# Performance work log

Measured on AMD Instinct MI355X. Metric: run time of the kernel, lower is better.

The kernel has to match this reference:

```python
import jax, jax.numpy as jnp
import numpy as np

N_HD, N_DEL7, N_AVP, N_AVM = 100, 100, 50, 50
DT = 0.001
KAPPA_PHI, KAPPA_Y = 1.0, 1.0
AV_OFFSET = 0.0
ALPHA_TILDE = 10.0
# alpha used in the leak term inside forward():
ALPHA = ALPHA_TILDE + 0.5 * KAPPA_Y / KAPPA_PHI * 1.0 / (KAPPA_PHI + KAPPA_Y)  # 10.25
W_HD_HD_S = ALPHA_TILDE + 1.0 / (KAPPA_PHI + KAPPA_Y) - AV_OFFSET * KAPPA_Y / (KAPPA_Y + KAPPA_PHI)  # 10.5
W_HD_AV_S = np.sqrt(2.0) * KAPPA_Y / (KAPPA_Y + KAPPA_PHI)  # sqrt(2)/2
W_HD_D7_S = 1.0 / (KAPPA_PHI + KAPPA_Y)  # 0.5
W_AV_HD_S = 1.0
W_D7_HD_S = 1.0
TAU_AV = 0.01
TAU_D7 = 0.001


def _id_matr(x_to, x_from, sig):
    d = np.arccos(np.cos(x_to[:, None] - x_from[None, :]))
    M = np.exp(-0.5 * (d / sig) ** 2) / (np.sqrt(2.0 * np.pi) * sig)
    return M / M.sum(1)[0]


def _build_weights():
    p_hd = np.linspace(-np.pi, np.pi - 2 * np.pi / N_HD, N_HD)
    p_d7 = np.linspace(-np.pi, np.pi - 2 * np.pi / N_DEL7, N_DEL7)
    p_avp = np.linspace(-np.pi, np.pi - 2 * np.pi / N_AVP, N_AVP)
    p_avm = np.linspace(-np.pi, np.pi - 2 * np.pi / N_AVM, N_AVM)
    o, w0, w1 = -0.2, 0.0, 2.0
    W_HD_HD = 2.0 / N_HD * (o + np.maximum(0.0, w0 + w1 * np.cos(p_hd[:, None] - p_hd[None, :])))
    W_HD_AVplus = 2.0 / N_AVP * np.maximum(0.0, np.sin(p_hd[:, None] - p_avp[None, :] + np.pi / 4))
    W_HD_AVminus = 2.0 / N_AVM * np.maximum(0.0, -np.sin(p_hd[:, None] - p_avm[None, :] - np.pi / 4))
    W_AVplus_HD = _id_matr(p_avp, p_hd, 0.3)
    W_AVminus_HD = _id_matr(p_avm, p_hd, 0.3)
    d7w0, d7w1 = 0.5, -0.5
    W_Del7_HD = 2.0 / N_DEL7 * (d7w0 + d7w1 * np.cos(p_d7[:, None] - p_hd[None, :]))
    m0, m1 = 0.1, 0.0
    W_Del7_Del7 = 2.0 / N_DEL7 * (m0 + m1 * np.cos(p_d7[:, None] - p_d7[None, :]))
    j = np.pi / 2 * (1 - 2 * m0) / d7w0
    W_HD_Del7 = -j * _id_matr(p_hd, p_d7, 0.1)
    ws = dict(W_HD_HD=W_HD_HD, W_HD_AVplus=W_HD_AVplus, W_HD_AVminus=W_HD_AVminus,
              W_AVplus_HD=W_AVplus_HD, W_AVminus_HD=W_AVminus_HD,
              W_Del7_HD=W_Del7_HD, W_Del7_Del7=W_Del7_Del7, W_HD_Del7=W_HD_Del7)
    return {k: jnp.asarray(v, dtype=jnp.float32) for k, v in ws.items()}


def setup_inputs() -> dict:
    key = jax.random.key(0)
    k1, k2 = jax.random.split(key)
    B, S = 64, 5000
    inp = {
        'inputs': jax.random.normal(k1, (B, S, 2), dtype=jnp.float32),
        'r0': jax.random.uniform(k2, (1, B, N_HD + N_AVP + N_AVM + N_DEL7), dtype=jnp.float32),
    }
    inp.update(_build_weights())
    return inp


def reference(inputs, r0, W_HD_HD, W_HD_AVplus, W_HD_AVminus, W_AVplus_HD,
              W_AVminus_HD, W_Del7_HD, W_Del7_Del7, W_HD_Del7):
    # batch_first -> [seq, batch, 2]
    x = jnp.transpose(inputs, (1, 0, 2))
    r_HD0 = r0[0, :, :N_HD]
    r_AVp0 = r0[0, :, N_HD:N_HD + N_AVP]
    r_AVm0 = r0[0, :, N_HD + N_AVP:N_HD + N_AVP + N_AVM]
    r_D70 = r0[0, :, N_HD + N_AVP + N_AVM:]
    relu = jax.nn.relu

    def step(carry, x_t):
        r_HD, r_AVp, r_AVm, r_D7 = carry
        av = x_t[:, 1]  # [B]; HD input only feeds a dead input_term in the original
        r_HD_new = (r_HD
                    - ALPHA * r_HD * DT
                    + W_HD_HD_S * jnp.einsum('ij,bj->bi', W_HD_HD, r_HD) * DT
                    + W_HD_AV_S * jnp.einsum('ij,bj->bi', W_HD_AVplus, r_AVp) * DT
                    + W_HD_AV_S * jnp.einsum('ij,bj->bi', W_HD_AVminus, r_AVm) * DT
                    + W_HD_D7_S * jnp.einsum('ij,bj->bi', W_HD_Del7, relu(r_D7)) * r_HD * DT)
        gate_p = (av / DT + AV_OFFSET)[:, None]
        gate_m = (-av / DT + AV_OFFSET)[:, None]
        r_AVp_new = r_AVp + (1.0 / TAU_AV) * (-r_AVp + gate_p * W_AV_HD_S * jnp.einsum('ij,bj->bi', W_AVplus_HD, r_HD_new)) * DT
        r_AVm_new = r_AVm + (1.0 / TAU_AV) * (-r_AVm + gate_m * W_AV_HD_S * jnp.einsum('ij,bj->bi', W_AVminus_HD, r_HD_new)) * DT
        r_D7_new = r_D7 + (1.0 / TAU_D7) * (-r_D7
                                            + W_D7_HD_S * jnp.einsum('ij,bj->bi', W_Del7_HD, relu(r_HD_new))
                                            + jnp.einsum('ij,bj->bi', W_Del7_Del7, relu(r_D7))) * DT
        out = jnp.concatenate([r_HD_new, r_AVp_new, r_AVm_new, r_D7_new], axis=1)  # [B, 300]
        return (r_HD_new, r_AVp_new, r_AVm_new, r_D7_new), out

    carry, ys = jax.lax.scan(step, (r_HD0, r_AVp0, r_AVm0, r_D70), x)
    output = jnp.transpose(ys, (1, 0, 2))  # [B, S, 300] (batch_first)
    r_full_curr = jnp.concatenate(carry, axis=1)
    return output, r_full_curr
```

## Files before the change

kernel.cpp:

```cpp
#include <hip/hip_runtime.h>


#define SSTEPS 5000
#define PI_D 3.14159265358979323846

template<int CTRL, int RM, bool BC>
__device__ __forceinline__ float dpp_mov_f(float x) {
  return __int_as_float(__builtin_amdgcn_update_dpp(0, __float_as_int(x), CTRL, RM, 0xF, BC));
}
__device__ __forceinline__ float scan16(float x) {
  x += dpp_mov_f<0x111, 0xF, true>(x);
  x += dpp_mov_f<0x112, 0xF, true>(x);
  x += dpp_mov_f<0x114, 0xF, true>(x);
  x += dpp_mov_f<0x118, 0xF, true>(x);
  return x;
}
__device__ __forceinline__ float scan8(float x) {
  x += dpp_mov_f<0x111, 0xF, true>(x);
  x += dpp_mov_f<0x112, 0xF, true>(x);
  x += dpp_mov_f<0x114, 0xF, true>(x);
  return x;
}
__device__ __forceinline__ float wave_sum(float x) {
  x = scan16(x);
  x += dpp_mov_f<0x142, 0xA, false>(x);
  x += dpp_mov_f<0x143, 0xC, false>(x);
  return __int_as_float(__builtin_amdgcn_readlane(__float_as_int(x), 63));
}

__global__ __launch_bounds__(1024, 4) void drosoph_rnn_kernel(
    const float* __restrict__ xin,
    const float* __restrict__ r0,
    const float* __restrict__ W_HD_HD,
    const float* __restrict__ W_HD_AVp,
    const float* __restrict__ W_HD_AVm,
    const float* __restrict__ W_AVp_HD,
    const float* __restrict__ W_AVm_HD,
    const float* __restrict__ W_D7_HD,
    const float* __restrict__ W_D7_D7,
    const float* __restrict__ W_HD_D7,
    float* __restrict__ out)
{
  const int b = blockIdx.x;
  const int t = threadIdx.x;

  __shared__ __align__(16) float su[2][328];
  __shared__ float avb[SSTEPS];
  __shared__ float d7r[104];

  const bool p1  = (t < 800);
  const int  g   = t >> 4;
  const int  r1  = t & 15;
  const bool pav = (t < 400);
  const int  a   = t >> 3;
  const int  qa  = t & 7;
  const bool pd7 = (t >= 832) && (t < 960);
  const int  dl  = t & 63;
  const int  o7  = t - 832;
  const bool pst = (t >= 960);

  float w1[2][20];
  if (p1) {
    #pragma unroll
    for (int k = 0; k < 2; ++k) {
      const int o = g + 50*k;
      #pragma unroll
      for (int q = 0; q < 20; ++q) {
        const int j = 20*r1 + q;
        float w;
        if      (j < 100) w = 10.5f                   * W_HD_HD [o*100 + j];
        else if (j < 150) w = 0.70710678118654752f    * W_HD_AVp[o*50 + (j-100)];
        else if (j < 200) w = 0.70710678118654752f    * W_HD_AVm[o*50 + (j-150)];
        else if (j < 300) w = 0.5f                    * W_HD_D7 [o*100 + (j-200)];
        else w = 0.0f;
        w1[k][q] = w;
      }
    }
  }

  float wav[16];
  if (pav) {
    #pragma unroll
    for (int u = 0; u < 4; ++u) {
      const int j0 = 4*(qa + 8*u);
      #pragma unroll
      for (int m = 0; m < 4; ++m) {
        const int j = j0 + m;
        wav[4*u+m] = (j < 100) ? W_AVp_HD[a*100 + j] : 0.0f;
      }
    }
  }

  float cw0=0.f, cw1=0.f, sw0=0.f, sw1=0.f, m0w=0.f, m1w=0.f, cd=0.f, sd=0.f;
  if (pd7) {
    const int j0 = 2*dl, j1 = 2*dl + 1;
    double pj0 = -PI_D + j0*(2.0*PI_D/100.0);
    double pj1 = -PI_D + j1*(2.0*PI_D/100.0);
    m0w = (j0 < 100) ? 1.0f : 0.0f;
    m1w = (j1 < 100) ? 1.0f : 0.0f;
    cw0 = m0w * (float)cos(pj0);  sw0 = m0w * (float)sin(pj0);
    cw1 = m1w * (float)cos(pj1);  sw1 = m1w * (float)sin(pj1);
    double po = -PI_D + o7*(2.0*PI_D/100.0);
    cd = (float)cos(po);  sd = (float)sin(po);
  }

  if (t < 328) { su[0][t] = 0.f; su[1][t] = 0.f; }
  if (t < 104) d7r[t] = 0.f;
  {
    const float2* x2 = (const float2*)xin + (size_t)b * SSTEPS;
    for (int i = t; i < SSTEPS; i += 1024) avb[i] = x2[i].y;
  }
  if (t < 300) {
    float v = r0[b*300 + t];
    su[0][t] = (t < 200) ? v : fmaxf(v, 0.f);
  }
  __syncthreads();

  float* outb = out + (size_t)b * ((size_t)SSTEPS * 300);
  int p = 0;

  #pragma unroll 1
  for (int s = 0; s < SSTEPS; ++s) {
    const float* suc = su[p];
    float*       sun = su[p^1];

    if (p1) {
      float vv[20];
      {
        const float4* vp = (const float4*)(suc + 20*r1);
        float4 q0=vp[0], q1=vp[1], q2=vp[2], q3=vp[3], q4=vp[4];
        *(float4*)&vv[0]=q0; *(float4*)&vv[4]=q1; *(float4*)&vv[8]=q2;
        *(float4*)&vv[12]=q3; *(float4*)&vv[16]=q4;
      }
      float hd0 = suc[g], hd1 = suc[g+50];
      float x0a=0.f, x0b=0.f, x1a=0.f, x1b=0.f;
      #pragma unroll
      for (int q = 0; q < 20; q += 2) {
        x0a = fmaf(w1[0][q],   vv[q],   x0a);
        x0b = fmaf(w1[0][q+1], vv[q+1], x0b);
        x1a = fmaf(w1[1][q],   vv[q],   x1a);
        x1b = fmaf(w1[1][q+1], vv[q+1], x1b);
      }
      float e0 = x0a + x0b, e1 = x1a + x1b;
      if (r1 >= 10) { e0 *= hd0; e1 *= hd1; }
      e0 = scan16(e0);
      e1 = scan16(e1);
      if (r1 == 15) {
        float h0 = fmaf(0.001f, fmaf(-10.25f, hd0, e0), hd0);
        float h1 = fmaf(0.001f, fmaf(-10.25f, hd1, e1), hd1);
        sun[g]    = h0;
        sun[g+50] = h1;
      }
    } else if (pst) {
      if (s > 0) {
        float* od = outb + (size_t)(s-1) * 300;
        #pragma unroll
        for (int u = 0; u < 5; ++u) {
          int idx = dl + 64*u;
          if (idx < 300) od[idx] = (idx < 200) ? suc[idx] : d7r[idx-200];
        }
      }
    }
    __syncthreads();

    if (pav) {
      const float4* hp = (const float4*)sun;
      float hh[16];
      *(float4*)&hh[0]  = hp[qa];
      *(float4*)&hh[4]  = hp[qa+8];
      *(float4*)&hh[8]  = hp[qa+16];
      *(float4*)&hh[12] = hp[qa+24];
      float da=0.f, db=0.f;
      #pragma unroll
      for (int m = 0; m < 16; m += 2) {
        da = fmaf(wav[m],   hh[m],   da);
        db = fmaf(wav[m+1], hh[m+1], db);
      }
      float d = scan8(da + db);
      if (qa == 7) {
        float av   = avb[s];
        float gp   = av / 0.001f;
        float gm   = -gp;
        float oldp = suc[100+a], oldm = suc[150+a];
        float np_  = fmaf(0.1f, fmaf(gp, d, -oldp), oldp);
        float nm_  = fmaf(0.1f, fmaf(gm, d, -oldm), oldm);
        sun[100+a] = np_;
        sun[150+a] = nm_;
      }
    }

    if (pd7) {
      float2 y2 = *(const float2*)(sun + 2*dl);
      float2 z2 = *(const float2*)(suc + 200 + 2*dl);
      float y0 = fmaxf(y2.x, 0.f), y1 = fmaxf(y2.y, 0.f);
      float pS0 = fmaf(m1w, y1,   m0w * y0);
      float pC  = fmaf(cw1, y1,   cw0 * y0);
      float pS  = fmaf(sw1, y1,   sw0 * y0);
      float pT  = fmaf(m1w, z2.y, m0w * z2.x);
      float S0 = wave_sum(pS0);
      float C  = wave_sum(pC);
      float S  = wave_sum(pS);
      float T0 = wave_sum(pT);
      if (o7 < 100) {
        float d7 = fmaf(0.002f, T0, 0.01f * (S0 - fmaf(cd, C, sd * S)));
        sun[200+o7] = fmaxf(d7, 0.f);
        d7r[o7]     = d7;
      }
    }
    __syncthreads();
    p ^= 1;
  }

  if (t < 300) {
    float v = (t < 200) ? su[p][t] : d7r[t-200];
    outb[(size_t)(SSTEPS-1) * 300 + t] = v;
    out[(size_t)64 * SSTEPS * 300 + (size_t)b * 300 + t] = v;
  }
}

extern "C" void kernel_launch(void* const* d_in, const int* in_sizes, int n_in,
                              void* d_out, int out_size, void* d_ws, size_t ws_size,
                              hipStream_t stream) {
  drosoph_rnn_kernel<<<64, 1024, 0, stream>>>(
      (const float*)d_in[0],
      (const float*)d_in[1],
      (const float*)d_in[2],
      (const float*)d_in[3],
      (const float*)d_in[4],
      (const float*)d_in[5],
      (const float*)d_in[6],
      (const float*)d_in[7],
      (const float*)d_in[8],
      (const float*)d_in[9],
      (float*)d_out);
}
```

Measured before the change: 3.979 ms.

## Move Del7 reductions off the critical path and prefetch HD state early

The HD-producing lanes now compute partial relu sums, cosine-weighted sums and sine-weighted sums of the new HD values. They reduce these by shuffles into a small shared buffer before the first barrier. As a result, the Del7 waves only combine 13 partials per quantity after the barrier instead of running four full wave reductions. The T0 reduction over previous Del7 state is moved before the first barrier as well. The HD state needed for the next step (hd and the first 100 values) is preloaded after the second phase, and the FMA chains are split into four accumulators. The extra shuffles and shared writes in phase one add some work to that phase in exchange for a shorter second phase.

After: 5.808 ms. +46.0%, slower.

```diff
diff --git a/kernel.cpp b/kernel.cpp
--- a/kernel.cpp
+++ b/kernel.cpp
@@ -9,23 +9,26 @@
   return __int_as_float(__builtin_amdgcn_update_dpp(0, __float_as_int(x), CTRL, RM, 0xF, BC));
 }
 __device__ __forceinline__ float scan16(float x) {
-  x += dpp_mov_f<0x111, 0xF, true>(x);
-  x += dpp_mov_f<0x112, 0xF, true>(x);
-  x += dpp_mov_f<0x114, 0xF, true>(x);
-  x += dpp_mov_f<0x118, 0xF, true>(x);
+  x += dpp_mov_f<0x111,0xF,true>(x);
+  x += dpp_mov_f<0x112,0xF,true>(x);
+  x += dpp_mov_f<0x114,0xF,true>(x);
+  x += dpp_mov_f<0x118,0xF,true>(x);
   return x;
 }
 __device__ __forceinline__ float scan8(float x) {
-  x += dpp_mov_f<0x111, 0xF, true>(x);
-  x += dpp_mov_f<0x112, 0xF, true>(x);
-  x += dpp_mov_f<0x114, 0xF, true>(x);
+  x += dpp_mov_f<0x111,0xF,true>(x);
+  x += dpp_mov_f<0x112,0xF,true>(x);
+  x += dpp_mov_f<0x114,0xF,true>(x);
   return x;
 }
 __device__ __forceinline__ float wave_sum(float x) {
   x = scan16(x);
-  x += dpp_mov_f<0x142, 0xA, false>(x);
-  x += dpp_mov_f<0x143, 0xC, false>(x);
+  x += dpp_mov_f<0x142,0xA,false>(x);
+  x += dpp_mov_f<0x143,0xC,false>(x);
   return __int_as_float(__builtin_amdgcn_readlane(__float_as_int(x), 63));
+}
+__device__ __forceinline__ float bcast_lane(float x, int l) {
+  return __int_as_float(__builtin_amdgcn_readlane(__float_as_int(x), l));
 }
 
 __global__ __launch_bounds__(1024, 4) void drosoph_rnn_kernel(
@@ -41,12 +44,15 @@
     const float* __restrict__ W_HD_D7,
     float* __restrict__ out)
 {
-  const int b = blockIdx.x;
-  const int t = threadIdx.x;
+  const int b    = blockIdx.x;
+  const int t    = threadIdx.x;
+  const int lane = t & 63;
+  const int wid  = t >> 6;
 
   __shared__ __align__(16) float su[2][328];
   __shared__ float avb[SSTEPS];
   __shared__ float d7r[104];
+  __shared__ float pbuf[48];
 
   const bool p1  = (t < 800);
   const int  g   = t >> 4;
@@ -54,10 +60,9 @@
   const bool pav = (t < 400);
   const int  a   = t >> 3;
   const int  qa  = t & 7;
-  const bool pd7 = (t >= 832) && (t < 960);
-  const int  dl  = t & 63;
-  const int  o7  = t - 832;
-  const bool pst = (t >= 960);
+  const bool d7w = (wid == 13) || (wid == 14);
+  const int  o7  = (wid - 13) * 64 + lane;
+  const bool pst = (wid == 15);
 
   float w1[2][20];
   if (p1) {
@@ -68,10 +73,10 @@
       for (int q = 0; q < 20; ++q) {
         const int j = 20*r1 + q;
         float w;
-        if      (j < 100) w = 10.5f                   * W_HD_HD [o*100 + j];
-        else if (j < 150) w = 0.70710678118654752f    * W_HD_AVp[o*50 + (j-100)];
-        else if (j < 200) w = 0.70710678118654752f    * W_HD_AVm[o*50 + (j-150)];
-        else if (j < 300) w = 0.5f                    * W_HD_D7 [o*100 + (j-200)];
+        if      (j < 100) w = 10.5f                * W_HD_HD [o*100 + j];
+        else if (j < 150) w = 0.70710678118654752f * W_HD_AVp[o*50 + (j-100)];
+        else if (j < 200) w = 0.70710678118654752f * W_HD_AVm[o*50 + (j-150)];
+        else if (j < 300) w = 0.5f                 * W_HD_D7 [o*100 + (j-200)];
         else w = 0.0f;
         w1[k][q] = w;
       }
@@ -91,17 +96,15 @@
     }
   }
 
-  float cw0=0.f, cw1=0.f, sw0=0.f, sw1=0.f, m0w=0.f, m1w=0.f, cd=0.f, sd=0.f;
-  if (pd7) {
-    const int j0 = 2*dl, j1 = 2*dl + 1;
-    double pj0 = -PI_D + j0*(2.0*PI_D/100.0);
-    double pj1 = -PI_D + j1*(2.0*PI_D/100.0);
-    m0w = (j0 < 100) ? 1.0f : 0.0f;
-    m1w = (j1 < 100) ? 1.0f : 0.0f;
-    cw0 = m0w * (float)cos(pj0);  sw0 = m0w * (float)sin(pj0);
-    cw1 = m1w * (float)cos(pj1);  sw1 = m1w * (float)sin(pj1);
-    double po = -PI_D + o7*(2.0*PI_D/100.0);
-    cd = (float)cos(po);  sd = (float)sin(po);
+  float cg = 0.f, sg = 0.f;
+  if (p1 && r1 == 15) {
+    double pg = -PI_D + g * (2.0 * PI_D / 100.0);
+    cg = (float)cos(pg); sg = (float)sin(pg);
+  }
+  float cd = 0.f, sd = 0.f;
+  if (d7w) {
+    double po = -PI_D + o7 * (2.0 * PI_D / 100.0);
+    cd = (float)cos(po); sd = (float)sin(po);
   }
 
   if (t < 328) { su[0][t] = 0.f; su[1][t] = 0.f; }
@@ -116,6 +119,16 @@
   }
   __syncthreads();
 
+  float4 pre0, pre1, pre2, pre3, pre4;
+  float hd0p = 0.f, hd1p = 0.f;
+  if (p1) {
+    hd0p = su[0][g]; hd1p = su[0][g+50];
+    if (r1 < 5) {
+      const float4* vp = (const float4*)(su[0] + 20*r1);
+      pre0 = vp[0]; pre1 = vp[1]; pre2 = vp[2]; pre3 = vp[3]; pre4 = vp[4];
+    }
+  }
+
   float* outb = out + (size_t)b * ((size_t)SSTEPS * 300);
   int p = 0;
 
@@ -123,25 +136,27 @@
   for (int s = 0; s < SSTEPS; ++s) {
     const float* suc = su[p];
     float*       sun = su[p^1];
+    float q0 = 0.f, q1 = 0.f, q2 = 0.f;
+    float T0loc = 0.f;
 
     if (p1) {
-      float vv[20];
-      {
+      float4 V0, V1, V2, V3, V4;
+      if (r1 < 5) { V0=pre0; V1=pre1; V2=pre2; V3=pre3; V4=pre4; }
+      else {
         const float4* vp = (const float4*)(suc + 20*r1);
-        float4 q0=vp[0], q1=vp[1], q2=vp[2], q3=vp[3], q4=vp[4];
-        *(float4*)&vv[0]=q0; *(float4*)&vv[4]=q1; *(float4*)&vv[8]=q2;
-        *(float4*)&vv[12]=q3; *(float4*)&vv[16]=q4;
-      }
-      float hd0 = suc[g], hd1 = suc[g+50];
-      float x0a=0.f, x0b=0.f, x1a=0.f, x1b=0.f;
-      #pragma unroll
-      for (int q = 0; q < 20; q += 2) {
-        x0a = fmaf(w1[0][q],   vv[q],   x0a);
-        x0b = fmaf(w1[0][q+1], vv[q+1], x0b);
-        x1a = fmaf(w1[1][q],   vv[q],   x1a);
-        x1b = fmaf(w1[1][q+1], vv[q+1], x1b);
-      }
-      float e0 = x0a + x0b, e1 = x1a + x1b;
+        V0=vp[0]; V1=vp[1]; V2=vp[2]; V3=vp[3]; V4=vp[4];
+      }
+      float hd0 = hd0p, hd1 = hd1p;
+      float xa0=0,xb0=0,xc0=0,xd0=0, xa1=0,xb1=0,xc1=0,xd1=0;
+      #define ACC4(BASE, V) \
+        xa0 = fmaf(w1[0][BASE+0], V.x, xa0); xb0 = fmaf(w1[0][BASE+1], V.y, xb0); \
+        xc0 = fmaf(w1[0][BASE+2], V.z, xc0); xd0 = fmaf(w1[0][BASE+3], V.w, xd0); \
+        xa1 = fmaf(w1[1][BASE+0], V.x, xa1); xb1 = fmaf(w1[1][BASE+1], V.y, xb1); \
+        xc1 = fmaf(w1[1][BASE+2], V.z, xc1); xd1 = fmaf(w1[1][BASE+3], V.w, xd1);
+      ACC4(0,  V0) ACC4(4,  V1) ACC4(8,  V2) ACC4(12, V3) ACC4(16, V4)
+      #undef ACC4
+      float e0 = (xa0+xb0)+(xc0+xd0);
+      float e1 = (xa1+xb1)+(xc1+xd1);
       if (r1 >= 10) { e0 *= hd0; e1 *= hd1; }
       e0 = scan16(e0);
       e1 = scan16(e1);
@@ -150,61 +165,74 @@
         float h1 = fmaf(0.001f, fmaf(-10.25f, hd1, e1), hd1);
         sun[g]    = h0;
         sun[g+50] = h1;
-      }
+        float rh0 = fmaxf(h0, 0.f), rh1 = fmaxf(h1, 0.f);
+        q0 = rh0 + rh1;
+        float dr = rh0 - rh1;
+        q1 = cg * dr;
+        q2 = sg * dr;
+      }
+    } else if (d7w) {
+      float x = 0.f;
+      if (lane < 50) { float2 z = *(const float2*)(suc + 200 + 2*lane); x = z.x + z.y; }
+      T0loc = wave_sum(x);
     } else if (pst) {
       if (s > 0) {
         float* od = outb + (size_t)(s-1) * 300;
         #pragma unroll
         for (int u = 0; u < 5; ++u) {
-          int idx = dl + 64*u;
+          int idx = lane + 64*u;
           if (idx < 300) od[idx] = (idx < 200) ? suc[idx] : d7r[idx-200];
         }
       }
     }
+    if (t < 832) {
+      q0 += __shfl_xor(q0, 16); q1 += __shfl_xor(q1, 16); q2 += __shfl_xor(q2, 16);
+      q0 += __shfl_xor(q0, 32); q1 += __shfl_xor(q1, 32); q2 += __shfl_xor(q2, 32);
+      if (lane == 15) { pbuf[wid] = q0; pbuf[16+wid] = q1; pbuf[32+wid] = q2; }
+    }
     __syncthreads();
 
     if (pav) {
       const float4* hp = (const float4*)sun;
-      float hh[16];
-      *(float4*)&hh[0]  = hp[qa];
-      *(float4*)&hh[4]  = hp[qa+8];
-      *(float4*)&hh[8]  = hp[qa+16];
-      *(float4*)&hh[12] = hp[qa+24];
-      float da=0.f, db=0.f;
-      #pragma unroll
-      for (int m = 0; m < 16; m += 2) {
-        da = fmaf(wav[m],   hh[m],   da);
-        db = fmaf(wav[m+1], hh[m+1], db);
-      }
-      float d = scan8(da + db);
+      float4 H0 = hp[qa], H1 = hp[qa+8], H2 = hp[qa+16], H3 = hp[qa+24];
+      float da=0,db=0,dc=0,dd=0;
+      da = fmaf(wav[0],  H0.x, da); db = fmaf(wav[1],  H0.y, db);
+      dc = fmaf(wav[2],  H0.z, dc); dd = fmaf(wav[3],  H0.w, dd);
+      da = fmaf(wav[4],  H1.x, da); db = fmaf(wav[5],  H1.y, db);
+      dc = fmaf(wav[6],  H1.z, dc); dd = fmaf(wav[7],  H1.w, dd);
+      da = fmaf(wav[8],  H2.x, da); db = fmaf(wav[9],  H2.y, db);
+      dc = fmaf(wav[10], H2.z, dc); dd = fmaf(wav[11], H2.w, dd);
+      da = fmaf(wav[12], H3.x, da); db = fmaf(wav[13], H3.y, db);
+      dc = fmaf(wav[14], H3.z, dc); dd = fmaf(wav[15], H3.w, dd);
+      float d = scan8((da+db)+(dc+dd));
       if (qa == 7) {
         float av   = avb[s];
         float gp   = av / 0.001f;
-        float gm   = -gp;
         float oldp = suc[100+a], oldm = suc[150+a];
-        float np_  = fmaf(0.1f, fmaf(gp, d, -oldp), oldp);
-        float nm_  = fmaf(0.1f, fmaf(gm, d, -oldm), oldm);
+        float np_  = fmaf(0.1f, fmaf(gp,  d, -oldp), oldp);
+        float nm_  = fmaf(0.1f, fmaf(-gp, d, -oldm), oldm);
         sun[100+a] = np_;
         sun[150+a] = nm_;
       }
     }
-
-    if (pd7) {
-      float2 y2 = *(const float2*)(sun + 2*dl);
-      float2 z2 = *(const float2*)(suc + 200 + 2*dl);
-      float y0 = fmaxf(y2.x, 0.f), y1 = fmaxf(y2.y, 0.f);
-      float pS0 = fmaf(m1w, y1,   m0w * y0);
-      float pC  = fmaf(cw1, y1,   cw0 * y0);
-      float pS  = fmaf(sw1, y1,   sw0 * y0);
-      float pT  = fmaf(m1w, z2.y, m0w * z2.x);
-      float S0 = wave_sum(pS0);
-      float C  = wave_sum(pC);
-      float S  = wave_sum(pS);
-      float T0 = wave_sum(pT);
+    if (d7w) {
+      int qq = lane >> 4, mm = lane & 15;
+      float v = (qq < 3 && mm < 13) ? pbuf[qq*16 + mm] : 0.f;
+      v = scan16(v);
+      float S0v = bcast_lane(v, 15);
+      float Cv  = bcast_lane(v, 31);
+      float Sv  = bcast_lane(v, 47);
       if (o7 < 100) {
-        float d7 = fmaf(0.002f, T0, 0.01f * (S0 - fmaf(cd, C, sd * S)));
+        float d7 = fmaf(0.002f, T0loc, 0.01f * (S0v - fmaf(cd, Cv, sd * Sv)));
         sun[200+o7] = fmaxf(d7, 0.f);
         d7r[o7]     = d7;
+      }
+    }
+    if (p1) {
+      hd0p = sun[g]; hd1p = sun[g+50];
+      if (r1 < 5) {
+        const float4* vp = (const float4*)(sun + 20*r1);
+        pre0 = vp[0]; pre1 = vp[1]; pre2 = vp[2]; pre3 = vp[3]; pre4 = vp[4];
       }
     }
     __syncthreads();
```
